# Kernel optimization log

Hardware: AMD Instinct MI355X
Metric: run time of the kernel (lower is better)

## Reference

```python
import jax, jax.numpy as jnp
import numpy as np

N_LAYERS = 4
EPS = 1e-5  # eqx.nn.LayerNorm default


def _kernels(lam, P, B, C, step, L):
    # Annotated-S4 DPLR generating-function kernel (Q = P), vectorized over H channels.
    # lam, P, B, C: (H, N) complex64; step: (H, 1) real. Returns K: (H, L) real.
    omega = jnp.exp((-2j * jnp.pi) * (jnp.arange(L) / L))            # (L,) roots of unity
    g = (2.0 / step) * ((1.0 - omega) / (1.0 + omega))[None, :]      # (H, L) bilinear warp
    c = 2.0 / (1.0 + omega)                                          # (L,)

    def cauchy(v):  # v: (H, N) -> (H, L): sum_n v_n / (g - lambda_n)
        return jnp.sum(v[:, None, :] / (g[:, :, None] - lam[:, None, :]), axis=-1)

    k00 = cauchy(jnp.conj(C) * B)
    k01 = cauchy(jnp.conj(C) * P)
    k10 = cauchy(jnp.conj(P) * B)
    k11 = cauchy(jnp.conj(P) * P)
    at_roots = c[None, :] * (k00 - k01 * (1.0 / (1.0 + k11)) * k10)  # woodbury correction
    return jnp.fft.ifft(at_roots, n=L, axis=-1).real                 # (H, L)


def _causal_conv(u, K):
    # u: (B, L, H) real input, K: (H, L) real kernel -> causal conv along L via zero-padded FFT.
    L = u.shape[1]
    Ud = jnp.fft.rfft(u, n=2 * L, axis=1)                 # (B, F, H)
    Kd = jnp.fft.rfft(K, n=2 * L, axis=-1)                # (H, F)
    return jnp.fft.irfft(Ud * Kd.T[None], n=2 * L, axis=1)[:, :L]


def _forward(x, enc_w, enc_b, dec_w, dec_b, lam_re, lam_im, p_re, p_im, b_re, b_im,
             c_re, c_im, d, log_step, norm_w, norm_b, w1, b1, w2, b2):
    L = x.shape[1]
    h = x @ enc_w.T + enc_b                               # encoder: (B, L, H)
    for i in range(N_LAYERS):
        skip = h
        mu = h.mean(-1, keepdims=True)
        var = ((h - mu) ** 2).mean(-1, keepdims=True)
        hn = (h - mu) / jnp.sqrt(var + EPS) * norm_w[i] + norm_b[i]
        K = _kernels(lam_re[i] + 1j * lam_im[i], p_re[i] + 1j * p_im[i],
                     b_re[i] + 1j * b_im[i], c_re[i] + 1j * c_im[i],
                     jnp.exp(log_step[i])[:, None], L)
        y = _causal_conv(hn, K) + hn * d[i]               # SSM conv + skip-through D term
        y = jax.nn.gelu(y)
        y = (y @ w1[i].T + b1[i]) * jax.nn.sigmoid(y @ w2[i].T + b2[i])  # gated MLP
        h = skip + y
    return h @ dec_w.T + dec_b                            # decoder: (B, L, out)


def setup_inputs() -> dict:
    key = jax.random.key(0)
    B, L, IN, OUT, H, N, NL = 8, 2048, 64, 64, 128, 64, N_LAYERS
    ks = jax.random.split(key, 12)
    rn = lambda k, s, sc: (jax.random.normal(k, s) * sc).astype(jnp.float32)
    return dict(
        x=rn(ks[0], (B, L, IN), 1.0),
        convolve=1,
        enc_w=rn(ks[1], (H, IN), 1.0 / np.sqrt(IN)), enc_b=jnp.zeros((H,), jnp.float32),
        dec_w=rn(ks[2], (OUT, H), 1.0 / np.sqrt(H)), dec_b=jnp.zeros((OUT,), jnp.float32),
        lam_re=-0.5 * jnp.ones((NL, H, N), jnp.float32),  # HiPPO/S4D-style stable poles
        lam_im=jnp.tile(jnp.float32(np.pi) * jnp.arange(N, dtype=jnp.float32), (NL, H, 1)),
        p_re=rn(ks[3], (NL, H, N), 0.5 / np.sqrt(N)), p_im=rn(ks[4], (NL, H, N), 0.5 / np.sqrt(N)),
        b_re=rn(ks[5], (NL, H, N), 1.0), b_im=rn(ks[6], (NL, H, N), 1.0),
        c_re=rn(ks[7], (NL, H, N), 1.0 / np.sqrt(N)), c_im=rn(ks[8], (NL, H, N), 1.0 / np.sqrt(N)),
        d=jnp.ones((NL, H), jnp.float32),
        log_step=(jax.random.uniform(ks[9], (NL, H)) * (np.log(0.1) - np.log(0.001))
                  + np.log(0.001)).astype(jnp.float32),
        norm_w=jnp.ones((NL, H), jnp.float32), norm_b=jnp.zeros((NL, H), jnp.float32),
        w1=rn(ks[10], (NL, H, H), 1.0 / np.sqrt(H)), b1=jnp.zeros((NL, H), jnp.float32),
        w2=rn(ks[11], (NL, H, H), 1.0 / np.sqrt(H)), b2=jnp.zeros((NL, H), jnp.float32),
    )


def reference(x, convolve, enc_w, enc_b, dec_w, dec_b, lam_re, lam_im, p_re, p_im,
              b_re, b_im, c_re, c_im, d, log_step, norm_w, norm_b, w1, b1, w2, b2):
    # convolve is static 1 (True): the FFT-convolution path of the S4 Model.
    return _forward(x, enc_w, enc_b, dec_w, dec_b, lam_re, lam_im, p_re, p_im, b_re, b_im,
                    c_re, c_im, d, log_step, norm_w, norm_b, w1, b1, w2, b2)
```

## Files before the change

### kernel.cpp

```cpp
#include <hip/hip_runtime.h>
#include <hip/hip_bf16.h>


#define Bsz 8
#define Lseq 2048
#define Hdim 128
#define Npol 64
#define NLAYERS 4

typedef __bf16 bf16x8 __attribute__((ext_vector_type(8)));
typedef float f32x16 __attribute__((ext_vector_type(16)));

__device__ __forceinline__ float fast_rcp(float x) { return __builtin_amdgcn_rcpf(x); }
__device__ __forceinline__ float fast_rsq(float x) { return __builtin_amdgcn_rsqf(x); }

__device__ __forceinline__ float2 cmulf(float2 a, float2 b) {
    return make_float2(a.x * b.x - a.y * b.y, a.x * b.y + a.y * b.x);
}
__device__ __forceinline__ float2 cmulc(float2 a, float2 b) {
    return make_float2(a.x * b.x + a.y * b.y, a.y * b.x - a.x * b.y);
}
__device__ __forceinline__ float2 cadd(float2 a, float2 b) {
    return make_float2(a.x + b.x, a.y + b.y);
}
__device__ __forceinline__ float2 csub(float2 a, float2 b) {
    return make_float2(a.x - b.x, a.y - b.y);
}

__device__ __forceinline__ float gelu_f(float v) {
    float z = 0.7978845608028654f * (v + 0.044715f * v * v * v);
    float e = __expf(2.0f * z);
    return v - v * fast_rcp(e + 1.0f);
}

__device__ __forceinline__ int sw(int i) { return (i & ~15) | ((i ^ (i >> 4)) & 15); }
__device__ __forceinline__ int ap(int i) { return i + (i >> 3); }
__device__ __forceinline__ int dr8(int p) {
    return ((p & 7) << 9) | (((p >> 3) & 7) << 6) | (((p >> 6) & 7) << 3) | (p >> 9);
}

static __device__ const float W16R[8] = {1.f, 0.9238795325f, 0.7071067812f, 0.3826834324f,
                                         0.f, -0.3826834324f, -0.7071067812f, -0.9238795325f};
static __device__ const float W16I[8] = {0.f, -0.3826834324f, -0.7071067812f, -0.9238795325f,
                                         -1.f, -0.9238795325f, -0.7071067812f, -0.3826834324f};
static __device__ const int BR4[16] = {0, 8, 4, 12, 2, 10, 6, 14, 1, 9, 5, 13, 3, 11, 7, 15};
static __device__ const int BR3[8] = {0, 4, 2, 6, 1, 5, 3, 7};

__device__ __forceinline__ float2 twget(const float2* __restrict__ tw, int e) {
    float2 w = tw[e & 2047];
    if (e & 2048) { w.x = -w.x; w.y = -w.y; }
    return w;
}

#define RC8 0.70710678118654752f
template <bool INV>
__device__ __forceinline__ float2 rotI(float2 z) {
    return INV ? make_float2(-z.y, z.x) : make_float2(z.y, -z.x);
}
template <bool INV>
__device__ __forceinline__ float2 rotW(float2 z) {
    return INV ? make_float2(RC8 * (z.x - z.y), RC8 * (z.x + z.y))
               : make_float2(RC8 * (z.x + z.y), RC8 * (z.y - z.x));
}
template <bool INV>
__device__ __forceinline__ float2 rotW3(float2 z) {
    return INV ? make_float2(-RC8 * (z.x + z.y), RC8 * (z.x - z.y))
               : make_float2(RC8 * (z.y - z.x), -RC8 * (z.x + z.y));
}

template <bool INV>
__device__ __forceinline__ void bfly8(float2 v[8]) {
    float2 a0 = cadd(v[0], v[4]), a1 = cadd(v[1], v[5]);
    float2 a2 = cadd(v[2], v[6]), a3 = cadd(v[3], v[7]);
    float2 b0 = csub(v[0], v[4]), b1 = csub(v[1], v[5]);
    float2 b2 = csub(v[2], v[6]), b3 = csub(v[3], v[7]);
    float2 c1 = rotW<INV>(b1), c2 = rotI<INV>(b2), c3 = rotW3<INV>(b3);
    float2 e0 = cadd(a0, a2), e1 = csub(a0, a2);
    float2 e2 = cadd(a1, a3), e3 = rotI<INV>(csub(a1, a3));
    v[0] = cadd(e0, e2); v[4] = csub(e0, e2);
    v[2] = cadd(e1, e3); v[6] = csub(e1, e3);
    float2 o0 = cadd(b0, c2), o1 = csub(b0, c2);
    float2 o2 = cadd(c1, c3), o3 = rotI<INV>(csub(c1, c3));
    v[1] = cadd(o0, o2); v[5] = csub(o0, o2);
    v[3] = cadd(o1, o3); v[7] = csub(o1, o3);
}

__device__ __forceinline__ void bfly8_hz(float2 v[8]) {
    float2 x0 = v[0], x1 = v[1], x2 = v[2], x3 = v[3];
    float2 c1 = rotW<false>(x1), c2 = rotI<false>(x2), c3 = rotW3<false>(x3);
    float2 e0 = cadd(x0, x2), e1 = csub(x0, x2);
    float2 e2 = cadd(x1, x3), e3 = rotI<false>(csub(x1, x3));
    v[0] = cadd(e0, e2); v[4] = csub(e0, e2);
    v[2] = cadd(e1, e3); v[6] = csub(e1, e3);
    float2 o0 = cadd(x0, c2), o1 = csub(x0, c2);
    float2 o2 = cadd(c1, c3), o3 = rotI<false>(csub(c1, c3));
    v[1] = cadd(o0, o2); v[5] = csub(o0, o2);
    v[3] = cadd(o1, o3); v[7] = csub(o1, o3);
}

template <bool INV>
__device__ __forceinline__ void fft16_dif(float2 v[16]) {
#pragma unroll
    for (int mi = 0; mi < 4; mi++) {
        const int m = 8 >> mi;
#pragma unroll
        for (int g = 0; g < 16; g += 2 * m) {
#pragma unroll
            for (int j = 0; j < m; j++) {
                float wr = W16R[j << mi];
                float wi = INV ? -W16I[j << mi] : W16I[j << mi];
                float2 a = v[g + j], b = v[g + j + m];
                float dx = a.x - b.x, dy = a.y - b.y;
                v[g + j] = make_float2(a.x + b.x, a.y + b.y);
                v[g + j + m] = make_float2(dx * wr - dy * wi, dx * wi + dy * wr);
            }
        }
    }
}

template <bool INV>
__device__ __forceinline__ void fft8_dif(float2 v[8]) {
#pragma unroll
    for (int mi = 0; mi < 3; mi++) {
        const int m = 4 >> mi;
#pragma unroll
        for (int g = 0; g < 8; g += 2 * m) {
#pragma unroll
            for (int j = 0; j < m; j++) {
                float wr = W16R[j << (mi + 1)];
                float wi = INV ? -W16I[j << (mi + 1)] : W16I[j << (mi + 1)];
                float2 a = v[g + j], b = v[g + j + m];
                float dx = a.x - b.x, dy = a.y - b.y;
                v[g + j] = make_float2(a.x + b.x, a.y + b.y);
                v[g + j + m] = make_float2(dx * wr - dy * wi, dx * wi + dy * wr);
            }
        }
    }
}

__device__ __forceinline__ void fft4096_passA_hz(float2* data, const float2* __restrict__ tw,
                                                 int t, const float2 vin[8]) {
    float2 v[16];
#pragma unroll
    for (int j = 0; j < 8; j++) v[j] = vin[j];
#pragma unroll
    for (int j = 0; j < 8; j++)
        v[j + 8] = cmulf(v[j], make_float2(W16R[j], W16I[j]));
#pragma unroll
    for (int mi = 1; mi < 4; mi++) {
        const int m = 8 >> mi;
#pragma unroll
        for (int g = 0; g < 16; g += 2 * m) {
#pragma unroll
            for (int j = 0; j < m; j++) {
                float wr = W16R[j << mi], wi = W16I[j << mi];
                float2 a = v[g + j], b = v[g + j + m];
                float dx = a.x - b.x, dy = a.y - b.y;
                v[g + j] = make_float2(a.x + b.x, a.y + b.y);
                v[g + j + m] = make_float2(dx * wr - dy * wi, dx * wi + dy * wr);
            }
        }
    }
#pragma unroll
    for (int i = 1; i < 16; i++) v[i] = cmulf(v[i], twget(tw, t * BR4[i]));
#pragma unroll
    for (int i = 0; i < 16; i++) data[sw(i * 256 + t)] = v[i];
}

__device__ __forceinline__ void fft4096_fwd_BC(float2* data, const float2* __restrict__ tw, int t) {
    __syncthreads();
    {
        int j0 = t & 15;
        int base = (t >> 4) * 256 + j0;
        float2 v[16];
#pragma unroll
        for (int k = 0; k < 16; k++) v[k] = data[sw(base + 16 * k)];
        fft16_dif<false>(v);
#pragma unroll
        for (int i = 1; i < 16; i++) v[i] = cmulf(v[i], twget(tw, 16 * j0 * BR4[i]));
#pragma unroll
        for (int i = 0; i < 16; i++) data[sw(base + 16 * i)] = v[i];
    }
    __syncthreads();
    {
        float2 v[16];
#pragma unroll
        for (int k = 0; k < 16; k++) v[k] = data[sw(t * 16 + k)];
        fft16_dif<false>(v);
#pragma unroll
        for (int i = 0; i < 16; i++) data[sw(t * 16 + i)] = v[i];
    }
    __syncthreads();
}

__device__ __forceinline__ void kfft_core(int hh, int t, float* smem,
                                          float2* __restrict__ KdL,
                                          const float2* __restrict__ tw,
                                          const float* __restrict__ lam_re,
                                          const float* __restrict__ lam_im,
                                          const float* __restrict__ p_re,
                                          const float* __restrict__ p_im,
                                          const float* __restrict__ b_re,
                                          const float* __restrict__ b_im,
                                          const float* __restrict__ c_re,
                                          const float* __restrict__ c_im,
                                          const float* __restrict__ log_step) {
    float2* data = (float2*)smem;
    float* ktmp = smem + 8192;
    float4* polA = (float4*)(smem + 10240);
    float4* polB = (float4*)(smem + 10496);
    float* n11S = smem + 10752;
    int baseP = hh * Npol;
    if (t < Npol) {
        int n = t;
        float lr = lam_re[baseP + n], li = lam_im[baseP + n];
        float pr = p_re[baseP + n], pi = p_im[baseP + n];
        float br = b_re[baseP + n], bi = b_im[baseP + n];
        float cr = c_re[baseP + n], ci = c_im[baseP + n];
        polA[n] = make_float4(lr, li, cr * br + ci * bi, cr * bi - ci * br);
        polB[n] = make_float4(cr * pr + ci * pi, cr * pi - ci * pr,
                              pr * br + pi * bi, pr * bi - pi * br);
        n11S[n] = pr * pr + pi * pi;
    }
    __syncthreads();
    {
        float step = expf(log_step[hh]);
        float gs = 2.0f / step;
        float wrv[8], wiv[8];
        float gr[8], gi[8];
#pragma unroll
        for (int j = 0; j < 8; j++) {
            int l = t + 256 * j;
            float ang = -6.283185307179586f * (float)l / (float)Lseq;
            float wr = cosf(ang), wi = sinf(ang);
            wrv[j] = wr; wiv[j] = wi;
            float dr = 1.0f + wr, di = wi;
            float invd2 = fast_rcp(dr * dr + di * di);
            float nr = 1.0f - wr, ni = -wi;
            gr[j] = gs * (nr * dr + ni * di) * invd2;
            gi[j] = gs * (ni * dr - nr * di) * invd2;
        }
        float k00x[8], k00y[8], k01x[8], k01y[8];
        float k10x[8], k10y[8], k11x[8], k11y[8];
#pragma unroll
        for (int j = 0; j < 8; j++) {
            k00x[j] = 0.f; k00y[j] = 0.f; k01x[j] = 0.f; k01y[j] = 0.f;
            k10x[j] = 0.f; k10y[j] = 0.f; k11x[j] = 0.f; k11y[j] = 0.f;
        }
        for (int n = 0; n < Npol; n++) {
            float4 A = polA[n];
            float4 B = polB[n];
            float n11 = n11S[n];
#pragma unroll
            for (int j = 0; j < 8; j++) {
                float er = gr[j] - A.x, ei = gi[j] - A.y;
                float inv2 = fast_rcp(fmaf(er, er, ei * ei));
                float ir = er * inv2;
                float mi = ei * inv2;
                k00x[j] = fmaf(A.z, ir, fmaf(A.w, mi, k00x[j]));
                k00y[j] = fmaf(A.w, ir, fmaf(-A.z, mi, k00y[j]));
                k01x[j] = fmaf(B.x, ir, fmaf(B.y, mi, k01x[j]));
                k01y[j] = fmaf(B.y, ir, fmaf(-B.x, mi, k01y[j]));
                k10x[j] = fmaf(B.z, ir, fmaf(B.w, mi, k10x[j]));
                k10y[j] = fmaf(B.w, ir, fmaf(-B.z, mi, k10y[j]));
                k11x[j] = fmaf(n11, ir, k11x[j]);
                k11y[j] = fmaf(-n11, mi, k11y[j]);
            }
        }
#pragma unroll
        for (int j = 0; j < 8; j++) {
            int l = t + 256 * j;
            float dr = 1.0f + wrv[j], di = wiv[j];
            float invd2 = fast_rcp(dr * dr + di * di);
            float cr2 = 2.0f * dr * invd2, ci2 = -2.0f * di * invd2;
            float wr2 = 1.0f + k11x[j], wi2 = k11y[j];
            float w2inv = fast_rcp(fmaf(wr2, wr2, wi2 * wi2));
            float vr = wr2 * w2inv, vi = -wi2 * w2inv;
            float t1x = k01x[j] * k10x[j] - k01y[j] * k10y[j];
            float t1y = k01x[j] * k10y[j] + k01y[j] * k10x[j];
            float t2x = t1x * vr - t1y * vi, t2y = t1x * vi + t1y * vr;
            float ex = k00x[j] - t2x, ey = k00y[j] - t2y;
            data[sw(l)] = make_float2(cr2 * ex - ci2 * ey, cr2 * ey + ci2 * ex);
        }
    }
    __syncthreads();
    if (t < 128) {
        float2 v[16];
#pragma unroll
        for (int k = 0; k < 16; k++) v[k] = data[sw(t + 128 * k)];
        fft16_dif<true>(v);
#pragma unroll
        for (int i = 1; i < 16; i++) v[i] = cmulc(v[i], twget(tw, 2 * t * BR4[i]));
#pragma unroll
        for (int i = 0; i < 16; i++) data[sw(i * 128 + t)] = v[i];
    }
    __syncthreads();
    if (t < 128) {
        int i2 = t >> 3, j0 = t & 7;
        int base2 = i2 * 128 + j0;
        float2 v[16];
#pragma unroll
        for (int k = 0; k < 16; k++) v[k] = data[sw(base2 + 8 * k)];
        fft16_dif<true>(v);
#pragma unroll
        for (int i = 1; i < 16; i++) v[i] = cmulc(v[i], twget(tw, 32 * j0 * BR4[i]));
#pragma unroll
        for (int i = 0; i < 16; i++) data[sw(base2 + 8 * i)] = v[i];
    }
    __syncthreads();
    {
        float2 v8[8];
#pragma unroll
        for (int k = 0; k < 8; k++) v8[k] = data[sw(t * 8 + k)];
        fft8_dif<true>(v8);
        int r = BR4[t >> 4], s = BR4[t & 15];
#pragma unroll
        for (int i = 0; i < 8; i++) {
            int l = r + 16 * s + 256 * BR3[i];
            ktmp[l] = v8[i].x * (1.0f / 2048.0f);
        }
    }
    __syncthreads();
    {
        float2 vin[8];
#pragma unroll
        for (int k = 0; k < 8; k++) vin[k] = make_float2(ktmp[t + 256 * k], 0.f);
        fft4096_passA_hz(data, tw, t, vin);
    }
    fft4096_fwd_BC(data, tw, t);
    float2* dst = KdL + (size_t)hh * 4096;
#pragma unroll
    for (int k = 0; k < 16; k++) {
        int p = t + 256 * k;
        int kf = dr8(p);
        int q = 256 * BR4[kf & 15] + 16 * BR4[(kf >> 4) & 15] + BR4[kf >> 8];
        dst[p] = data[sw(q)];
    }
}

__global__ __launch_bounds__(256, 4) void prep_kernel(const float* __restrict__ w1,
                                                      const float* __restrict__ w2,
                                                      const float* __restrict__ dec_w,
                                                      const float* __restrict__ enc_w,
                                                      float2* __restrict__ tw,
                                                      __bf16* __restrict__ wbf,
                                                      __bf16* __restrict__ decbf,
                                                      __bf16* __restrict__ encbf) {
    int bid = blockIdx.x, t = threadIdx.x;
    if (bid < 8) {
        int k = bid * 256 + t;
        if (k < 2048) {
            double a = -6.283185307179586476925286766559 * (double)k / 4096.0;
            tw[k] = make_float2((float)cos(a), (float)sin(a));
        }
        return;
    }
    if (bid < 264) {
        int i = (bid - 8) * 256 + t;
        int layer = i >> 14, rem = i & 16383;
        wbf[((size_t)layer * 2) * 16384 + rem] = (__bf16)w1[i];
        wbf[((size_t)layer * 2 + 1) * 16384 + rem] = (__bf16)w2[i];
        return;
    }
    if (bid < 296) {
        int i = (bid - 264) * 256 + t;
        decbf[i] = (__bf16)dec_w[i];
        return;
    }
    int i = (bid - 296) * 256 + t;
    encbf[i] = (__bf16)enc_w[i];
}

__global__ __launch_bounds__(256) void kfft_enc_kernel(float2* __restrict__ Kd1,
                                                       const float2* __restrict__ tw,
                                                       const float* __restrict__ x,
                                                       const __bf16* __restrict__ encbf,
                                                       const float* __restrict__ enc_b,
                                                       const float* __restrict__ nw,
                                                       const float* __restrict__ nb,
                                                       float* __restrict__ h,
                                                       float* __restrict__ hnT,
                                                       const float* __restrict__ lam_re,
                                                       const float* __restrict__ lam_im,
                                                       const float* __restrict__ p_re,
                                                       const float* __restrict__ p_im,
                                                       const float* __restrict__ b_re,
                                                       const float* __restrict__ b_im,
                                                       const float* __restrict__ c_re,
                                                       const float* __restrict__ c_im,
                                                       const float* __restrict__ log_step) {
    __shared__ __align__(16) float smem[10816];
    int bid = blockIdx.x, t = threadIdx.x;
    if (bid < 512) {
        int hh = bid & 127, layer = bid >> 7;
        int PN = Hdim * Npol;
        kfft_core(hh, t, smem, Kd1 + (size_t)layer * Hdim * 4096, tw,
                  lam_re + layer * PN, lam_im + layer * PN,
                  p_re + layer * PN, p_im + layer * PN,
                  b_re + layer * PN, b_im + layer * PN,
                  c_re + layer * PN, c_im + layer * PN,
                  log_step + layer * Hdim);
    } else {
        int r0 = (bid - 512) * 32;
        __bf16* ybf = (__bf16*)smem;
        float* dots = smem + 1152;
        float2* mv = (float2*)(smem + 5376);
        int bb = r0 >> 11, l0 = r0 & 2047;
        for (int i = t; i < 32 * 64; i += 256) {
            int r = i >> 6, k = i & 63;
            ybf[r * 72 + k] = (__bf16)x[(size_t)(r0 + r) * 64 + k];
        }
        __syncthreads();
        int wave = t >> 6, lane = t & 63;
        int m = lane & 31, half = lane >> 5;
        bf16x8 a[4];
#pragma unroll
        for (int kk = 0; kk < 4; kk++)
            a[kk] = *(const bf16x8*)&ybf[m * 72 + kk * 16 + half * 8];
        int o = 32 * wave + m;
        const __bf16* wr = encbf + (size_t)o * 64 + half * 8;
        f32x16 acc;
#pragma unroll
        for (int i = 0; i < 16; i++) acc[i] = 0.f;
#pragma unroll
        for (int kk = 0; kk < 4; kk++) {
            bf16x8 bw = *(const bf16x8*)(wr + kk * 16);
            acc = __builtin_amdgcn_mfma_f32_32x32x16_bf16(a[kk], bw, acc, 0, 0, 0);
        }
        float bo = enc_b[o];
#pragma unroll
        for (int reg = 0; reg < 16; reg++) {
            int row = (reg & 3) + 8 * (reg >> 2) + 4 * half;
            dots[row * 132 + o] = acc[reg] + bo;
        }
        __syncthreads();
        {
            int row = t >> 3, lane8 = t & 7;
            float s1 = 0.f, s2 = 0.f;
            int base = row * 132 + lane8 * 16;
#pragma unroll
            for (int q = 0; q < 4; q++) {
                float4 v4 = *(const float4*)&dots[base + 4 * q];
                s1 += v4.x + v4.y + v4.z + v4.w;
                s2 += v4.x * v4.x + v4.y * v4.y + v4.z * v4.z + v4.w * v4.w;
            }
#pragma unroll
            for (int mm = 1; mm < 8; mm <<= 1) { s1 += __shfl_xor(s1, mm); s2 += __shfl_xor(s2, mm); }
            if (lane8 == 0) {
                float mu = s1 * (1.0f / 128.0f);
                float var = s2 * (1.0f / 128.0f) - mu * mu;
                mv[row] = make_float2(mu, fast_rsq(var + 1e-5f));
            }
        }
        __syncthreads();
        {
            int o2 = t & 127, rh = t >> 7;
            float nwc = nw[o2], nbc = nb[o2];
            float hnv[16];
#pragma unroll
            for (int j = 0; j < 16; j++) {
                int r = rh * 16 + j;
                float hvv = dots[r * 132 + o2];
                h[(size_t)(r0 + r) * Hdim + o2] = hvv;
                float2 mvv = mv[r];
                hnv[j] = (hvv - mvv.x) * mvv.y * nwc + nbc;
            }
            float* dst = hnT + ((size_t)bb * Hdim + o2) * Lseq + l0 + rh * 16;
            *(float4*)(dst)      = make_float4(hnv[0],  hnv[1],  hnv[2],  hnv[3]);
            *(float4*)(dst + 4)  = make_float4(hnv[4],  hnv[5],  hnv[6],  hnv[7]);
            *(float4*)(dst + 8)  = make_float4(hnv[8],  hnv[9],  hnv[10], hnv[11]);
            *(float4*)(dst + 12) = make_float4(hnv[12], hnv[13], hnv[14], hnv[15]);
        }
    }
}

__global__ __launch_bounds__(512, 4) void conv_kernel(float* __restrict__ hnT,
                                                      const float2* __restrict__ Kd1,
                                                      const float* __restrict__ dvec,
                                                      const float2* __restrict__ tw) {
    int h = blockIdx.x, bp = blockIdx.y, t = threadIdx.x;
    __shared__ float2 data[4608];
    float* u0 = hnT + ((size_t)(2 * bp) * Hdim + h) * Lseq;
    float* u1 = hnT + ((size_t)(2 * bp + 1) * Hdim + h) * Lseq;
    float2 ureg[4];
    float2 Kreg[8];
    const float4* Kp4 = (const float4*)(Kd1 + (size_t)h * 4096 + t * 8);
    {
        float2 v[8];
#pragma unroll
        for (int k = 0; k < 4; k++) {
            int l = t + 512 * k;
            float2 u2 = make_float2(u0[l], u1[l]);
            ureg[k] = u2;
            v[k] = u2;
        }
#pragma unroll
        for (int k = 0; k < 4; k++) {
            float4 q = Kp4[k];
            Kreg[2 * k]     = make_float2(q.x, q.y);
            Kreg[2 * k + 1] = make_float2(q.z, q.w);
        }
        bfly8_hz(v);
#pragma unroll
        for (int r = 1; r < 8; r++) v[r] = cmulf(v[r], twget(tw, t * r));
#pragma unroll
        for (int r = 0; r < 8; r++) data[ap(r * 512 + t)] = v[r];
    }
    __syncthreads();
    {
        int j = t & 63;
        int base = (t >> 6) * 512 + j;
        float2 v[8];
#pragma unroll
        for (int m = 0; m < 8; m++) v[m] = data[ap(base + 64 * m)];
        bfly8<false>(v);
#pragma unroll
        for (int r = 1; r < 8; r++) v[r] = cmulf(v[r], twget(tw, 8 * j * r));
#pragma unroll
        for (int m = 0; m < 8; m++) data[ap(base + 64 * m)] = v[m];
    }
    __syncthreads();
    {
        int j = t & 7;
        int base = (t >> 3) * 64 + j;
        float2 v[8];
#pragma unroll
        for (int m = 0; m < 8; m++) v[m] = data[ap(base + 8 * m)];
        bfly8<false>(v);
#pragma unroll
        for (int r = 1; r < 8; r++) v[r] = cmulf(v[r], twget(tw, 64 * j * r));
#pragma unroll
        for (int m = 0; m < 8; m++) data[ap(base + 8 * m)] = v[m];
    }
    __syncthreads();
    {
        const float scale = 1.0f / 4096.0f;
        int base = t * 8;
        float2 v[8];
#pragma unroll
        for (int m = 0; m < 8; m++) v[m] = data[ap(base + m)];
        bfly8<false>(v);
#pragma unroll
        for (int r = 0; r < 8; r++) {
            float2 W = cmulf(v[r], Kreg[r]);
            v[r] = make_float2(W.x * scale, W.y * scale);
        }
        bfly8<true>(v);
#pragma unroll
        for (int m = 0; m < 8; m++) data[ap(base + m)] = v[m];
    }
    __syncthreads();
    {
        int j = t & 7;
        int base = (t >> 3) * 64 + j;
        float2 v[8];
#pragma unroll
        for (int m = 0; m < 8; m++) v[m] = data[ap(base + 8 * m)];
#pragma unroll
        for (int r = 1; r < 8; r++) v[r] = cmulc(v[r], twget(tw, 64 * j * r));
        bfly8<true>(v);
#pragma unroll
        for (int m = 0; m < 8; m++) data[ap(base + 8 * m)] = v[m];
    }
    __syncthreads();
    {
        int j = t & 63;
        int base = (t >> 6) * 512 + j;
        float2 v[8];
#pragma unroll
        for (int m = 0; m < 8; m++) v[m] = data[ap(base + 64 * m)];
#pragma unroll
        for (int r = 1; r < 8; r++) v[r] = cmulc(v[r], twget(tw, 8 * j * r));
        bfly8<true>(v);
#pragma unroll
        for (int m = 0; m < 8; m++) data[ap(base + 64 * m)] = v[m];
    }
    __syncthreads();
    {
        float2 v[8];
#pragma unroll
        for (int r = 0; r < 8; r++) v[r] = data[ap(r * 512 + t)];
#pragma unroll
        for (int r = 1; r < 8; r++) v[r] = cmulc(v[r], twget(tw, t * r));
        bfly8<true>(v);
        float dcoef = dvec[h];
#pragma unroll
        for (int k = 0; k < 4; k++) {
            int l = t + 512 * k;
            u0[l] = gelu_f(v[k].x + ureg[k].x * dcoef);
            u1[l] = gelu_f(v[k].y + ureg[k].y * dcoef);
        }
    }
}

__global__ __launch_bounds__(256) void mlp_kernel(const float* __restrict__ yT,
                                                  float* __restrict__ h,
                                                  float* __restrict__ hnT,
                                                  const __bf16* __restrict__ w1b,
                                                  const __bf16* __restrict__ w2b,
                                                  const float* __restrict__ b1,
                                                  const float* __restrict__ b2,
                                                  const float* __restrict__ nw,
                                                  const float* __restrict__ nb) {
    int r0 = blockIdx.x * 32;
    int t = threadIdx.x;
    int wave = t >> 6, lane = t & 63;
    __shared__ __align__(16) __bf16 ybf[32 * 136];
    __shared__ float dots[32 * 132];
    __shared__ float2 mv[32];
    int bb = r0 >> 11, l0 = r0 & 2047;
    for (int i = t; i < 32 * 128; i += 256) {
        int r = i & 31, k = i >> 5;
        ybf[r * 136 + k] = (__bf16)yT[((size_t)bb * Hdim + k) * Lseq + l0 + r];
    }
    __syncthreads();
    int m = lane & 31, half = lane >> 5;
    bf16x8 a[8];
#pragma unroll
    for (int kk = 0; kk < 8; kk++)
        a[kk] = *(const bf16x8*)&ybf[m * 136 + kk * 16 + half * 8];
    int out = 32 * wave + m;
    const __bf16* w1r = w1b + (size_t)out * 128 + half * 8;
    const __bf16* w2r = w2b + (size_t)out * 128 + half * 8;
    f32x16 acc1, acc2;
#pragma unroll
    for (int i = 0; i < 16; i++) { acc1[i] = 0.f; acc2[i] = 0.f; }
#pragma unroll
    for (int kk = 0; kk < 8; kk++) {
        bf16x8 bw1 = *(const bf16x8*)(w1r + kk * 16);
        bf16x8 bw2 = *(const bf16x8*)(w2r + kk * 16);
        acc1 = __builtin_amdgcn_mfma_f32_32x32x16_bf16(a[kk], bw1, acc1, 0, 0, 0);
        acc2 = __builtin_amdgcn_mfma_f32_32x32x16_bf16(a[kk], bw2, acc2, 0, 0, 0);
    }
    float bias1 = b1[out], bias2 = b2[out];
#pragma unroll
    for (int reg = 0; reg < 16; reg++) {
        int row = (reg & 3) + 8 * (reg >> 2) + 4 * half;
        float v1 = acc1[reg] + bias1;
        float v2 = acc2[reg] + bias2;
        float g = fast_rcp(1.0f + __expf(-v2));
        float hv = h[(size_t)(r0 + row) * Hdim + out] + v1 * g;
        dots[row * 132 + out] = hv;
    }
    __syncthreads();
    {
        int row = t >> 3, lane8 = t & 7;
        float s1 = 0.f, s2 = 0.f;
        int base = row * 132 + lane8 * 16;
#pragma unroll
        for (int q = 0; q < 4; q++) {
            float4 v4 = *(const float4*)&dots[base + 4 * q];
            s1 += v4.x + v4.y + v4.z + v4.w;
            s2 += v4.x * v4.x + v4.y * v4.y + v4.z * v4.z + v4.w * v4.w;
        }
#pragma unroll
        for (int mm = 1; mm < 8; mm <<= 1) { s1 += __shfl_xor(s1, mm); s2 += __shfl_xor(s2, mm); }
        if (lane8 == 0) {
            float mu = s1 * (1.0f / 128.0f);
            float var = s2 * (1.0f / 128.0f) - mu * mu;
            mv[row] = make_float2(mu, fast_rsq(var + 1e-5f));
        }
    }
    __syncthreads();
    {
        int o = t & 127, rh = t >> 7;
        float nwc = nw[o], nbc = nb[o];
        float hnv[16];
#pragma unroll
        for (int j = 0; j < 16; j++) {
            int r = rh * 16 + j;
            float hvv = dots[r * 132 + o];
            h[(size_t)(r0 + r) * Hdim + o] = hvv;
            float2 mvv = mv[r];
            hnv[j] = (hvv - mvv.x) * mvv.y * nwc + nbc;
        }
        float* dst = hnT + ((size_t)bb * Hdim + o) * Lseq + l0 + rh * 16;
        *(float4*)(dst)      = make_float4(hnv[0],  hnv[1],  hnv[2],  hnv[3]);
        *(float4*)(dst + 4)  = make_float4(hnv[4],  hnv[5],  hnv[6],  hnv[7]);
        *(float4*)(dst + 8)  = make_float4(hnv[8],  hnv[9],  hnv[10], hnv[11]);
        *(float4*)(dst + 12) = make_float4(hnv[12], hnv[13], hnv[14], hnv[15]);
    }
}

__global__ __launch_bounds__(256) void mlpdec_kernel(const float* __restrict__ yT,
                                                     const float* __restrict__ h,
                                                     const __bf16* __restrict__ w1b,
                                                     const __bf16* __restrict__ w2b,
                                                     const float* __restrict__ b1,
                                                     const float* __restrict__ b2,
                                                     const __bf16* __restrict__ decb,
                                                     const float* __restrict__ dec_bias,
                                                     float* __restrict__ out) {
    int r0 = blockIdx.x * 32;
    int t = threadIdx.x;
    int wave = t >> 6, lane = t & 63;
    __shared__ __align__(16) __bf16 ybf[32 * 136];
    __shared__ float dots[32 * 132];
    int bb = r0 >> 11, l0 = r0 & 2047;
    for (int i = t; i < 32 * 128; i += 256) {
        int r = i & 31, k = i >> 5;
        ybf[r * 136 + k] = (__bf16)yT[((size_t)bb * Hdim + k) * Lseq + l0 + r];
    }
    __syncthreads();
    int m = lane & 31, half = lane >> 5;
    bf16x8 a[8];
#pragma unroll
    for (int kk = 0; kk < 8; kk++)
        a[kk] = *(const bf16x8*)&ybf[m * 136 + kk * 16 + half * 8];
    int outc = 32 * wave + m;
    const __bf16* w1r = w1b + (size_t)outc * 128 + half * 8;
    const __bf16* w2r = w2b + (size_t)outc * 128 + half * 8;
    f32x16 acc1, acc2;
#pragma unroll
    for (int i = 0; i < 16; i++) { acc1[i] = 0.f; acc2[i] = 0.f; }
#pragma unroll
    for (int kk = 0; kk < 8; kk++) {
        bf16x8 bw1 = *(const bf16x8*)(w1r + kk * 16);
        bf16x8 bw2 = *(const bf16x8*)(w2r + kk * 16);
        acc1 = __builtin_amdgcn_mfma_f32_32x32x16_bf16(a[kk], bw1, acc1, 0, 0, 0);
        acc2 = __builtin_amdgcn_mfma_f32_32x32x16_bf16(a[kk], bw2, acc2, 0, 0, 0);
    }
    float bias1 = b1[outc], bias2 = b2[outc];
#pragma unroll
    for (int reg = 0; reg < 16; reg++) {
        int row = (reg & 3) + 8 * (reg >> 2) + 4 * half;
        float v1 = acc1[reg] + bias1;
        float v2 = acc2[reg] + bias2;
        float g = fast_rcp(1.0f + __expf(-v2));
        float hv = h[(size_t)(r0 + row) * Hdim + outc] + v1 * g;
        dots[row * 132 + outc] = hv;
    }
    __syncthreads();
    for (int i = t; i < 32 * 128; i += 256) {
        int r = i >> 7, k = i & 127;
        ybf[r * 136 + k] = (__bf16)dots[r * 132 + k];
    }
    __syncthreads();
    if (wave < 2) {
        bf16x8 a2[8];
#pragma unroll
        for (int kk = 0; kk < 8; kk++)
            a2[kk] = *(const bf16x8*)&ybf[m * 136 + kk * 16 + half * 8];
        int oc = 32 * wave + m;
        const __bf16* wr = decb + (size_t)oc * 128 + half * 8;
        f32x16 acc;
#pragma unroll
        for (int i = 0; i < 16; i++) acc[i] = 0.f;
#pragma unroll
        for (int kk = 0; kk < 8; kk++) {
            bf16x8 bw = *(const bf16x8*)(wr + kk * 16);
            acc = __builtin_amdgcn_mfma_f32_32x32x16_bf16(a2[kk], bw, acc, 0, 0, 0);
        }
        float bo = dec_bias[oc];
#pragma unroll
        for (int reg = 0; reg < 16; reg++) {
            int row = (reg & 3) + 8 * (reg >> 2) + 4 * half;
            out[(size_t)(r0 + row) * 64 + oc] = acc[reg] + bo;
        }
    }
}

extern "C" void kernel_launch(void* const* d_in, const int* in_sizes, int n_in,
                              void* d_out, int out_size, void* d_ws, size_t ws_size,
                              hipStream_t stream) {
    const float* x      = (const float*)d_in[0];
    const float* enc_w  = (const float*)d_in[2];
    const float* enc_b  = (const float*)d_in[3];
    const float* dec_w  = (const float*)d_in[4];
    const float* dec_b  = (const float*)d_in[5];
    const float* lam_re = (const float*)d_in[6];
    const float* lam_im = (const float*)d_in[7];
    const float* p_re   = (const float*)d_in[8];
    const float* p_im   = (const float*)d_in[9];
    const float* b_re   = (const float*)d_in[10];
    const float* b_im   = (const float*)d_in[11];
    const float* c_re   = (const float*)d_in[12];
    const float* c_im   = (const float*)d_in[13];
    const float* dvec   = (const float*)d_in[14];
    const float* lstep  = (const float*)d_in[15];
    const float* norm_w = (const float*)d_in[16];
    const float* norm_b = (const float*)d_in[17];
    const float* w1     = (const float*)d_in[18];
    const float* b1     = (const float*)d_in[19];
    const float* w2     = (const float*)d_in[20];
    const float* b2     = (const float*)d_in[21];
    float* out = (float*)d_out;

    char* ws = (char*)d_ws;
    float2* tw  = (float2*)ws;  ws += 2048 * sizeof(float2);
    float*  h   = (float*)ws;   ws += (size_t)Bsz * Lseq * Hdim * sizeof(float);
    float*  hnT = (float*)ws;   ws += (size_t)Bsz * Lseq * Hdim * sizeof(float);
    float2* Kd1 = (float2*)ws;  ws += (size_t)NLAYERS * Hdim * 4096 * sizeof(float2);
    __bf16* wbf = (__bf16*)ws;  ws += (size_t)NLAYERS * 2 * Hdim * Hdim * sizeof(__bf16);
    __bf16* dbf = (__bf16*)ws;  ws += (size_t)64 * Hdim * sizeof(__bf16);
    __bf16* ebf = (__bf16*)ws;  ws += (size_t)Hdim * 64 * sizeof(__bf16);

    const int nrows = Bsz * Lseq;

    prep_kernel<<<328, 256, 0, stream>>>(w1, w2, dec_w, enc_w, tw, wbf, dbf, ebf);
    kfft_enc_kernel<<<512 + nrows / 32, 256, 0, stream>>>(
        Kd1, tw, x, ebf, enc_b, norm_w, norm_b, h, hnT,
        lam_re, lam_im, p_re, p_im, b_re, b_im, c_re, c_im, lstep);
    for (int L = 0; L < NLAYERS; L++) {
        conv_kernel<<<dim3(Hdim, Bsz / 2), 512, 0, stream>>>(
            hnT, Kd1 + (size_t)L * Hdim * 4096, dvec + L * Hdim, tw);
        const __bf16* w1bL = wbf + (size_t)L * 2 * Hdim * Hdim;
        const __bf16* w2bL = w1bL + Hdim * Hdim;
        if (L < NLAYERS - 1) {
            const float* nwn = norm_w + (L + 1) * Hdim;
            const float* nbn = norm_b + (L + 1) * Hdim;
            mlp_kernel<<<nrows / 32, 256, 0, stream>>>(hnT, h, hnT, w1bL, w2bL,
                                                       b1 + L * Hdim, b2 + L * Hdim,
                                                       nwn, nbn);
        } else {
            mlpdec_kernel<<<nrows / 32, 256, 0, stream>>>(hnT, h, w1bL, w2bL,
                                                          b1 + L * Hdim, b2 + L * Hdim,
                                                          dbf, dec_b, out);
        }
    }
}
```

Measured before the change: 294.2 us.

## Replace paired-batch complex FFT conv with real-to-complex half-length FFT per batch

The causal convolution previously packed two batch rows into one 4096-point complex FFT. It now packs even and odd samples of a single row into a 2048-point complex FFT and uses the real-FFT split/merge identity (pw_pair) to multiply by the kernel spectrum. The launch becomes one block of 256 threads per (h, batch) with half the shared memory. The kernel spectrum output ordering and the kfft shared memory layout are adjusted to match. This removes about half the butterfly work and LDS traffic per row, at the cost of an extra radix-4 pass and more complex pointwise post-processing with a Nyquist special case.

```diff
diff --git a/kernel.cpp b/kernel.cpp
--- a/kernel.cpp
+++ b/kernel.cpp
@@ -34,9 +34,12 @@
 }
 
 __device__ __forceinline__ int sw(int i) { return (i & ~15) | ((i ^ (i >> 4)) & 15); }
-__device__ __forceinline__ int ap(int i) { return i + (i >> 3); }
-__device__ __forceinline__ int dr8(int p) {
-    return ((p & 7) << 9) | (((p >> 3) & 7) << 6) | (((p >> 6) & 7) << 3) | (p >> 9);
+__device__ __forceinline__ int sw2(int i) { return i ^ ((i >> 4) & 15); }
+__device__ __forceinline__ int slot2048(int k) {
+    return ((k & 7) << 8) | (((k >> 3) & 7) << 5) | (((k >> 6) & 7) << 2) | (k >> 9);
+}
+__device__ __forceinline__ int rev4(int x) {
+    return ((x & 1) << 3) | ((x & 2) << 1) | ((x & 4) >> 1) | ((x & 8) >> 3);
 }
 
 static __device__ const float W16R[8] = {1.f, 0.9238795325f, 0.7071067812f, 0.3826834324f,
@@ -99,6 +102,15 @@
 }
 
 template <bool INV>
+__device__ __forceinline__ void bfly4(float2 v[4]) {
+    float2 t0 = cadd(v[0], v[2]), t1 = csub(v[0], v[2]);
+    float2 t2 = cadd(v[1], v[3]), t3 = csub(v[1], v[3]);
+    float2 r3 = rotI<INV>(t3);
+    v[0] = cadd(t0, t2); v[2] = csub(t0, t2);
+    v[1] = cadd(t1, r3); v[3] = csub(t1, r3);
+}
+
+template <bool INV>
 __device__ __forceinline__ void fft16_dif(float2 v[16]) {
 #pragma unroll
     for (int mi = 0; mi < 4; mi++) {
@@ -206,10 +218,10 @@
                                           const float* __restrict__ c_im,
                                           const float* __restrict__ log_step) {
     float2* data = (float2*)smem;
+    float4* polA = (float4*)(smem + 8192);
+    float4* polB = (float4*)(smem + 8448);
+    float* n11S = smem + 8704;
     float* ktmp = smem + 8192;
-    float4* polA = (float4*)(smem + 10240);
-    float4* polB = (float4*)(smem + 10496);
-    float* n11S = smem + 10752;
     int baseP = hh * Npol;
     if (t < Npol) {
         int n = t;
@@ -332,8 +344,7 @@
 #pragma unroll
     for (int k = 0; k < 16; k++) {
         int p = t + 256 * k;
-        int kf = dr8(p);
-        int q = 256 * BR4[kf & 15] + 16 * BR4[(kf >> 4) & 15] + BR4[kf >> 8];
+        int q = (rev4(p & 15) << 8) | (rev4((p >> 4) & 15) << 4) | rev4(p >> 8);
         dst[p] = data[sw(q)];
     }
 }
@@ -389,7 +400,7 @@
                                                        const float* __restrict__ c_re,
                                                        const float* __restrict__ c_im,
                                                        const float* __restrict__ log_step) {
-    __shared__ __align__(16) float smem[10816];
+    __shared__ __align__(16) float smem[10240];
     int bid = blockIdx.x, t = threadIdx.x;
     if (bid < 512) {
         int hh = bid & 127, layer = bid >> 7;
@@ -474,121 +485,160 @@
     }
 }
 
-__global__ __launch_bounds__(512, 4) void conv_kernel(float* __restrict__ hnT,
-                                                      const float2* __restrict__ Kd1,
-                                                      const float* __restrict__ dvec,
-                                                      const float2* __restrict__ tw) {
-    int h = blockIdx.x, bp = blockIdx.y, t = threadIdx.x;
-    __shared__ float2 data[4608];
-    float* u0 = hnT + ((size_t)(2 * bp) * Hdim + h) * Lseq;
-    float* u1 = hnT + ((size_t)(2 * bp + 1) * Hdim + h) * Lseq;
+__device__ __forceinline__ void pw_pair(float2* data, const float2* __restrict__ tw,
+                                        int k, float2 Kdk, float2 Kdk2) {
+    const float s = 1.0f / 2048.0f;
+    int kp = (2048 - k) & 2047;
+    int s1 = sw2(slot2048(k));
+    int s2 = sw2(slot2048(kp));
+    float2 Zk = data[s1], Zp = data[s2];
+    float2 A = make_float2(0.5f * (Zk.x + Zp.x), 0.5f * (Zk.y - Zp.y));
+    float2 Bv = make_float2(0.5f * (Zk.y + Zp.y), 0.5f * (Zp.x - Zk.x));
+    float2 W = twget(tw, k);
+    float2 WB = cmulf(W, Bv);
+    float2 Up = cadd(A, WB);
+    float2 Um = csub(A, WB);
+    float2 Vp = cmulf(Up, Kdk);
+    float2 Vm = cmulf(Um, Kdk2);
+    float2 E = make_float2(0.5f * (Vp.x + Vm.x), 0.5f * (Vp.y + Vm.y));
+    float2 Dv = make_float2(0.5f * (Vp.x - Vm.x), 0.5f * (Vp.y - Vm.y));
+    float2 O = cmulc(Dv, W);
+    data[s1] = make_float2(s * (E.x - O.y), s * (E.y + O.x));
+    if (s2 != s1)
+        data[s2] = make_float2(s * (E.x + O.y), s * (O.x - E.y));
+}
+
+__global__ __launch_bounds__(256) void conv_kernel(float* __restrict__ hnT,
+                                                   const float2* __restrict__ Kd1,
+                                                   const float* __restrict__ dvec,
+                                                   const float2* __restrict__ tw) {
+    int h = blockIdx.x, b = blockIdx.y, t = threadIdx.x;
+    __shared__ float2 data[2048];
+    float* u0 = hnT + ((size_t)b * Hdim + h) * Lseq;
     float2 ureg[4];
     float2 Kreg[8];
-    const float4* Kp4 = (const float4*)(Kd1 + (size_t)h * 4096 + t * 8);
+    float2 Knyq0, Knyq1;
+    const float2* Kp = Kd1 + (size_t)h * 4096;
     {
         float2 v[8];
-#pragma unroll
-        for (int k = 0; k < 4; k++) {
-            int l = t + 512 * k;
-            float2 u2 = make_float2(u0[l], u1[l]);
-            ureg[k] = u2;
-            v[k] = u2;
-        }
-#pragma unroll
-        for (int k = 0; k < 4; k++) {
-            float4 q = Kp4[k];
-            Kreg[2 * k]     = make_float2(q.x, q.y);
-            Kreg[2 * k + 1] = make_float2(q.z, q.w);
-        }
+        const float2* up = (const float2*)u0;
+#pragma unroll
+        for (int r = 0; r < 4; r++) {
+            float2 z = up[t + 256 * r];
+            ureg[r] = z;
+            v[r] = z;
+        }
+#pragma unroll
+        for (int j = 0; j < 4; j++) {
+            Kreg[2 * j] = Kp[t + 256 * j];
+            Kreg[2 * j + 1] = Kp[t + 256 * j + 2048];
+        }
+        if (t == 0) { Knyq0 = Kp[1024]; Knyq1 = Kp[3072]; }
         bfly8_hz(v);
 #pragma unroll
-        for (int r = 1; r < 8; r++) v[r] = cmulf(v[r], twget(tw, t * r));
-#pragma unroll
-        for (int r = 0; r < 8; r++) data[ap(r * 512 + t)] = v[r];
-    }
-    __syncthreads();
-    {
-        int j = t & 63;
-        int base = (t >> 6) * 512 + j;
+        for (int m = 1; m < 8; m++) v[m] = cmulf(v[m], twget(tw, 2 * t * m));
+#pragma unroll
+        for (int m = 0; m < 8; m++) data[sw2(m * 256 + t)] = v[m];
+    }
+    __syncthreads();
+    {
+        int g = t >> 5, u5 = t & 31;
+        int base = g * 256 + u5;
         float2 v[8];
 #pragma unroll
-        for (int m = 0; m < 8; m++) v[m] = data[ap(base + 64 * m)];
+        for (int r = 0; r < 8; r++) v[r] = data[sw2(base + 32 * r)];
         bfly8<false>(v);
 #pragma unroll
-        for (int r = 1; r < 8; r++) v[r] = cmulf(v[r], twget(tw, 8 * j * r));
-#pragma unroll
-        for (int m = 0; m < 8; m++) data[ap(base + 64 * m)] = v[m];
-    }
-    __syncthreads();
-    {
-        int j = t & 7;
-        int base = (t >> 3) * 64 + j;
+        for (int m = 1; m < 8; m++) v[m] = cmulf(v[m], twget(tw, 16 * u5 * m));
+#pragma unroll
+        for (int m = 0; m < 8; m++) data[sw2(g * 256 + m * 32 + u5)] = v[m];
+    }
+    __syncthreads();
+    {
+        int c = t >> 2, q = t & 3;
+        int base = c * 32 + q;
         float2 v[8];
 #pragma unroll
-        for (int m = 0; m < 8; m++) v[m] = data[ap(base + 8 * m)];
+        for (int r = 0; r < 8; r++) v[r] = data[sw2(base + 4 * r)];
         bfly8<false>(v);
 #pragma unroll
-        for (int r = 1; r < 8; r++) v[r] = cmulf(v[r], twget(tw, 64 * j * r));
-#pragma unroll
-        for (int m = 0; m < 8; m++) data[ap(base + 8 * m)] = v[m];
-    }
-    __syncthreads();
-    {
-        const float scale = 1.0f / 4096.0f;
-        int base = t * 8;
+        for (int m = 1; m < 8; m++) v[m] = cmulf(v[m], twget(tw, 128 * q * m));
+#pragma unroll
+        for (int m = 0; m < 8; m++) data[sw2(c * 32 + m * 4 + q)] = v[m];
+    }
+    __syncthreads();
+    {
+#pragma unroll
+        for (int e = 0; e < 2; e++) {
+            int bidx = t + 256 * e;
+            float2 v[4];
+#pragma unroll
+            for (int d = 0; d < 4; d++) v[d] = data[sw2(4 * bidx + d)];
+            bfly4<false>(v);
+#pragma unroll
+            for (int d = 0; d < 4; d++) data[sw2(4 * bidx + d)] = v[d];
+        }
+    }
+    __syncthreads();
+    {
+#pragma unroll
+        for (int j = 0; j < 4; j++)
+            pw_pair(data, tw, t + 256 * j, Kreg[2 * j], Kreg[2 * j + 1]);
+        if (t == 0) pw_pair(data, tw, 1024, Knyq0, Knyq1);
+    }
+    __syncthreads();
+    {
+#pragma unroll
+        for (int e = 0; e < 2; e++) {
+            int bidx = t + 256 * e;
+            float2 v[4];
+#pragma unroll
+            for (int d = 0; d < 4; d++) v[d] = data[sw2(4 * bidx + d)];
+            bfly4<true>(v);
+#pragma unroll
+            for (int d = 0; d < 4; d++) data[sw2(4 * bidx + d)] = v[d];
+        }
+    }
+    __syncthreads();
+    {
+        int c = t >> 2, q = t & 3;
         float2 v[8];
 #pragma unroll
-        for (int m = 0; m < 8; m++) v[m] = data[ap(base + m)];
-        bfly8<false>(v);
-#pragma unroll
-        for (int r = 0; r < 8; r++) {
-            float2 W = cmulf(v[r], Kreg[r]);
-            v[r] = make_float2(W.x * scale, W.y * scale);
-        }
+        for (int m = 0; m < 8; m++) v[m] = data[sw2(c * 32 + m * 4 + q)];
+#pragma unroll
+        for (int m = 1; m < 8; m++) v[m] = cmulc(v[m], twget(tw, 128 * q * m));
         bfly8<true>(v);
 #pragma unroll
-        for (int m = 0; m < 8; m++) data[ap(base + m)] = v[m];
-    }
-    __syncthreads();
-    {
-        int j = t & 7;
-        int base = (t >> 3) * 64 + j;
+        for (int r = 0; r < 8; r++) data[sw2(c * 32 + q + 4 * r)] = v[r];
+    }
+    __syncthreads();
+    {
+        int g = t >> 5, u5 = t & 31;
         float2 v[8];
 #pragma unroll
-        for (int m = 0; m < 8; m++) v[m] = data[ap(base + 8 * m)];
-#pragma unroll
-        for (int r = 1; r < 8; r++) v[r] = cmulc(v[r], twget(tw, 64 * j * r));
+        for (int m = 0; m < 8; m++) v[m] = data[sw2(g * 256 + m * 32 + u5)];
+#pragma unroll
+        for (int m = 1; m < 8; m++) v[m] = cmulc(v[m], twget(tw, 16 * u5 * m));
         bfly8<true>(v);
 #pragma unroll
-        for (int m = 0; m < 8; m++) data[ap(base + 8 * m)] = v[m];
-    }
-    __syncthreads();
-    {
-        int j = t & 63;
-        int base = (t >> 6) * 512 + j;
+        for (int r = 0; r < 8; r++) data[sw2(g * 256 + u5 + 32 * r)] = v[r];
+    }
+    __syncthreads();
+    {
         float2 v[8];
 #pragma unroll
-        for (int m = 0; m < 8; m++) v[m] = data[ap(base + 64 * m)];
-#pragma unroll
-        for (int r = 1; r < 8; r++) v[r] = cmulc(v[r], twget(tw, 8 * j * r));
-        bfly8<true>(v);
-#pragma unroll
-        for (int m = 0; m < 8; m++) data[ap(base + 64 * m)] = v[m];
-    }
-    __syncthreads();
-    {
-        float2 v[8];
-#pragma unroll
-        for (int r = 0; r < 8; r++) v[r] = data[ap(r * 512 + t)];
-#pragma unroll
-        for (int r = 1; r < 8; r++) v[r] = cmulc(v[r], twget(tw, t * r));
+        for (int m = 0; m < 8; m++) v[m] = data[sw2(m * 256 + t)];
+#pragma unroll
+        for (int m = 1; m < 8; m++) v[m] = cmulc(v[m], twget(tw, 2 * t * m));
         bfly8<true>(v);
         float dcoef = dvec[h];
-#pragma unroll
-        for (int k = 0; k < 4; k++) {
-            int l = t + 512 * k;
-            u0[l] = gelu_f(v[k].x + ureg[k].x * dcoef);
-            u1[l] = gelu_f(v[k].y + ureg[k].y * dcoef);
+        float2* up = (float2*)u0;
+#pragma unroll
+        for (int r = 0; r < 4; r++) {
+            float2 w = v[r];
+            float2 uo = ureg[r];
+            up[t + 256 * r] = make_float2(gelu_f(w.x + uo.x * dcoef),
+                                          gelu_f(w.y + uo.y * dcoef));
         }
     }
 }
@@ -802,7 +852,7 @@
         Kd1, tw, x, ebf, enc_b, norm_w, norm_b, h, hnT,
         lam_re, lam_im, p_re, p_im, b_re, b_im, c_re, c_im, lstep);
     for (int L = 0; L < NLAYERS; L++) {
-        conv_kernel<<<dim3(Hdim, Bsz / 2), 512, 0, stream>>>(
+        conv_kernel<<<dim3(Hdim, Bsz), 256, 0, stream>>>(
             hnT, Kd1 + (size_t)L * Hdim * 4096, dvec + L * Hdim, tw);
         const __bf16* w1bL = wbf + (size_t)L * 2 * Hdim * Hdim;
         const __bf16* w2bL = w1bL + Hdim * Hdim;
```

Result: slower. 313.9 us (+6.7%).
